# Kernel optimization log

Hardware: AMD Instinct MI355X
Metric: run time of the kernel (lower is better)

The kernel has to match this reference:

```python
import jax, jax.numpy as jnp
import numpy as np

D_MODEL = 1024
NUM_HEADS = 16
D_K = D_MODEL // NUM_HEADS


def setup_inputs() -> dict:
    key = jax.random.key(0)
    ks = jax.random.split(key, 5)
    B, S = 4, 2048
    scale = 1.0 / np.sqrt(D_MODEL)
    return {
        "X": jax.random.normal(ks[0], (B, S, D_MODEL), dtype=jnp.float32),
        "W_q": jax.random.normal(ks[1], (D_MODEL, D_MODEL), dtype=jnp.float32) * scale,
        "W_k": jax.random.normal(ks[2], (D_MODEL, D_MODEL), dtype=jnp.float32) * scale,
        "W_v": jax.random.normal(ks[3], (D_MODEL, D_MODEL), dtype=jnp.float32) * scale,
        "W_h": jax.random.normal(ks[4], (D_MODEL, D_MODEL), dtype=jnp.float32) * scale,
        "b_h": jnp.zeros((D_MODEL,), dtype=jnp.float32),
    }


def reference(X, W_q, W_k, W_v, W_h, b_h):
    # X: [B, S, D] (batch_first=True). Linear weights stored [out, in] as in torch.
    B, S, _ = X.shape

    def split_heads(t):  # [B, S, D] -> [B, H, S, d_k]
        return t.reshape(B, S, NUM_HEADS, D_K).transpose(0, 2, 1, 3)

    Q = split_heads(jnp.einsum('bsd,od->bso', X, W_q))
    K = split_heads(jnp.einsum('bsd,od->bso', X, W_k))
    V = split_heads(jnp.einsum('bsd,od->bso', X, W_v))

    inv_sqrt_dk = jnp.asarray(1.0 / np.sqrt(D_K), dtype=X.dtype)
    scores = jnp.einsum('bhqd,bhkd->bhqk', Q * inv_sqrt_dk, K)  # [B,H,S,S]
    A = jax.nn.softmax(scores, axis=-1)
    H = jnp.einsum('bhqk,bhkd->bhqd', A, V)  # [B,H,S,d_k]
    H_cat = H.transpose(0, 2, 1, 3).reshape(B, S, D_MODEL)
    out = jnp.einsum('bsd,od->bso', H_cat, W_h) + b_h
    return out
```

## Files before the change

kernel.cpp:

```cpp
#include <hip/hip_runtime.h>
#include <hip/hip_bf16.h>


typedef short bf16x8 __attribute__((ext_vector_type(8)));
typedef short bf16x4 __attribute__((ext_vector_type(4)));
typedef float f32x4 __attribute__((ext_vector_type(4)));

#define D_MODEL 1024
#define SEQ     2048
#define BATCH   4
#define NHEAD   16
#define DK      64
#define LOG2E   1.44269504088896340736f
#define QSCALE  (0.125f * LOG2E)

__device__ __forceinline__ bf16x8 load8(const __hip_bfloat16* p) {
    return *reinterpret_cast<const bf16x8*>(p);
}
__device__ __forceinline__ short b16rne(float x) {
    unsigned u = __float_as_uint(x);
    u = (u + 0x7FFFu + ((u >> 16) & 1u)) >> 16;
    return (short)u;
}
__device__ __forceinline__ unsigned cvt_pk_bf16(float lo, float hi) {
    unsigned d;
    asm("v_cvt_pk_bf16_f32 %0, %1, %2" : "=v"(d) : "v"(lo), "v"(hi));
    return d;
}
__device__ __forceinline__ bf16x8 cvt8(const float* p) {
    f32x4 a = *reinterpret_cast<const f32x4*>(p);
    f32x4 b = *reinterpret_cast<const f32x4*>(p + 4);
    union { unsigned u[4]; bf16x8 v; } r;
    r.u[0] = cvt_pk_bf16(a[0], a[1]);
    r.u[1] = cvt_pk_bf16(a[2], a[3]);
    r.u[2] = cvt_pk_bf16(b[0], b[1]);
    r.u[3] = cvt_pk_bf16(b[2], b[3]);
    return r.v;
}
__device__ __forceinline__ void gld_lds16(const __hip_bfloat16* g, __hip_bfloat16* l) {
    __builtin_amdgcn_global_load_lds(
        (const __attribute__((address_space(1))) unsigned int*)g,
        (__attribute__((address_space(3))) unsigned int*)l, 16, 0, 0);
}

#define NX8 1048576
#define NW8 131072
__global__ __launch_bounds__(256) void cvt_all(
    const float* __restrict__ X,  const float* __restrict__ Wq,
    const float* __restrict__ Wk, const float* __restrict__ Wv,
    const float* __restrict__ Wh,
    __hip_bfloat16* __restrict__ Xb, __hip_bfloat16* __restrict__ Wqkv,
    __hip_bfloat16* __restrict__ Whb)
{
    int g = blockIdx.x * 256 + threadIdx.x;
    const float* src;
    __hip_bfloat16* dst;
    if (g < NX8) {
        src = X + (size_t)g * 8;
        dst = Xb + (size_t)g * 8;
    } else {
        int t = g - NX8;
        int r = t >> 17;
        int off = t & (NW8 - 1);
        const float* s0 = (r == 0) ? Wq : (r == 1) ? Wk : (r == 2) ? Wv : Wh;
        src = s0 + (size_t)off * 8;
        dst = ((r < 3) ? (Wqkv + (size_t)r * NW8 * 8) : Whb) + (size_t)off * 8;
    }
    *reinterpret_cast<bf16x8*>(dst) = cvt8(src);
}

__global__ __launch_bounds__(256) void qkv_gemm128(
    const __hip_bfloat16* __restrict__ Xb,
    const __hip_bfloat16* __restrict__ Wqkv,
    __hip_bfloat16* __restrict__ Qo,
    __hip_bfloat16* __restrict__ Ko,
    __hip_bfloat16* __restrict__ Vto)
{
    __shared__ __align__(16) __hip_bfloat16 At[128 * 32];
    __shared__ __align__(16) __hip_bfloat16 Bt[128 * 32];

    const int tid  = threadIdx.x;
    const int wave = tid >> 6, lane = tid & 63;
    const int l15  = lane & 15, quad = lane >> 4;
    const int wm   = wave >> 1, wn = wave & 1;
    const int bm0  = blockIdx.y * 128;
    const int bn0  = blockIdx.x * 128;

    const int srow = wave * 16 + (lane >> 2);
    const int scol = ((lane & 3) ^ ((lane >> 3) & 3)) * 8;
    const __hip_bfloat16* gA = Xb   + (size_t)(bm0 + srow) * 1024 + scol;
    const __hip_bfloat16* gB = Wqkv + (size_t)(bn0 + srow) * 1024 + scol;
    __hip_bfloat16* lA = At + wave * 512;
    __hip_bfloat16* lB = Bt + wave * 512;

    const int rsw = (l15 >> 1) & 3;

    f32x4 acc[4][4];
    #pragma unroll
    for (int i = 0; i < 4; ++i)
        #pragma unroll
        for (int j = 0; j < 4; ++j) acc[i][j] = (f32x4){0.f, 0.f, 0.f, 0.f};

    for (int k0 = 0; k0 < 1024; k0 += 32) {
        gld_lds16(gA + k0,                      lA);
        gld_lds16(gA + (size_t)64 * 1024 + k0,  lA + 2048);
        gld_lds16(gB + k0,                      lB);
        gld_lds16(gB + (size_t)64 * 1024 + k0,  lB + 2048);
        __syncthreads();

        bf16x8 af[4], bfr[4];
        #pragma unroll
        for (int i = 0; i < 4; ++i)
            af[i] = load8(At + (wm * 64 + i * 16 + l15) * 32 + ((quad ^ rsw) * 8));
        #pragma unroll
        for (int j = 0; j < 4; ++j)
            bfr[j] = load8(Bt + (wn * 64 + j * 16 + l15) * 32 + ((quad ^ rsw) * 8));
        #pragma unroll
        for (int i = 0; i < 4; ++i)
            #pragma unroll
            for (int j = 0; j < 4; ++j)
                acc[i][j] = __builtin_amdgcn_mfma_f32_16x16x32_bf16(af[i], bfr[j], acc[i][j], 0, 0, 0);
        __syncthreads();
    }

    const int z = bn0 >> 10;
    #pragma unroll
    for (int j = 0; j < 4; ++j) {
        int n  = bn0 + wn * 64 + j * 16 + l15;
        int nn = n & 1023;
        int h  = nn >> 6, d = nn & 63;
        #pragma unroll
        for (int i = 0; i < 4; ++i) {
            int m0 = bm0 + wm * 64 + i * 16 + quad * 4;
            int b  = m0 >> 11, s0 = m0 & 2047;
            if (z == 2) {
                uint2 pv;
                pv.x = cvt_pk_bf16(acc[i][j][0], acc[i][j][1]);
                pv.y = cvt_pk_bf16(acc[i][j][2], acc[i][j][3]);
                *reinterpret_cast<uint2*>(
                    &Vto[((size_t)((b << 4) + h) * DK + d) * SEQ + s0]) = pv;
            } else {
                #pragma unroll
                for (int r = 0; r < 4; ++r) {
                    float val = acc[i][j][r];
                    short v;
                    if (z == 0) v = b16rne(val * QSCALE); else v = b16rne(val);
                    __hip_bfloat16 bv = *reinterpret_cast<__hip_bfloat16*>(&v);
                    if (z == 0)
                        Qo[((size_t)((b << 4) + h) * SEQ + (s0 + r)) * DK + d] = bv;
                    else
                        Ko[((size_t)((b << 4) + h) * SEQ + (s0 + r)) * DK + d] = bv;
                }
            }
        }
    }
}

__global__ __launch_bounds__(256, 4) void flash_attn(
    const __hip_bfloat16* __restrict__ Q,
    const __hip_bfloat16* __restrict__ K,
    const __hip_bfloat16* __restrict__ Vt,
    __hip_bfloat16* __restrict__ H)
{
    __shared__ __align__(16) __hip_bfloat16 Kt[2][64 * 64];
    __shared__ __align__(16) __hip_bfloat16 Vs[64 * 64];
    __shared__ __align__(16) __hip_bfloat16 Plds[4][2][16][64];

    const int w    = threadIdx.x >> 6;
    const int lane = threadIdx.x & 63;
    const int l15  = lane & 15;
    const int quad = lane >> 4;
    const int x7   = l15 & 7;
    const int bh   = blockIdx.x & 63;
    const int b    = bh >> 4, h = bh & 15;
    const int q0   = (blockIdx.x >> 6) * 128 + w * 32;

    const __hip_bfloat16* Qb = Q  + (size_t)bh * SEQ * DK;
    const __hip_bfloat16* Kb = K  + (size_t)bh * SEQ * DK;
    const __hip_bfloat16* Vb = Vt + (size_t)bh * DK * SEQ;

    const int srsub = lane >> 3;
    const int sseg  = (lane & 7) ^ srsub;
    const int krow0 = w * 16 + srsub;
    const __hip_bfloat16* gK0 = Kb + (size_t)krow0 * DK + sseg * 8;
    const __hip_bfloat16* gK1 = Kb + (size_t)(krow0 + 8) * DK + sseg * 8;
    const __hip_bfloat16* gV0 = Vb + (size_t)krow0 * SEQ + sseg * 8;
    const __hip_bfloat16* gV1 = Vb + (size_t)(krow0 + 8) * SEQ + sseg * 8;
    __hip_bfloat16* lV0 = Vs + (w * 16) * 64;
    __hip_bfloat16* lV1 = Vs + (w * 16 + 8) * 64;

    bf16x8 qf[2][2];
    #pragma unroll
    for (int m = 0; m < 2; ++m)
        #pragma unroll
        for (int dh = 0; dh < 2; ++dh)
            qf[m][dh] = load8(Qb + (size_t)(q0 + m * 16 + l15) * DK + dh * 32 + quad * 8);

    bf16x8 onesf;
    #pragma unroll
    for (int j = 0; j < 8; ++j) onesf[j] = (short)0x3F80;

    f32x4 o[2][4];
    #pragma unroll
    for (int m = 0; m < 2; ++m)
        #pragma unroll
        for (int t = 0; t < 4; ++t) o[m][t] = (f32x4){0.f, 0.f, 0.f, 0.f};
    f32x4 lacc[2] = {{0.f,0.f,0.f,0.f}, {0.f,0.f,0.f,0.f}};

    gld_lds16(gK0, &Kt[0][(w * 16) * 64]);
    gld_lds16(gK1, &Kt[0][(w * 16 + 8) * 64]);
    __syncthreads();

    int cb = 0;
    for (int kv = 0; kv < SEQ; kv += 64) {
        const int nb  = cb ^ 1;
        const int kvn = (kv + 64) & (SEQ - 1);

        gld_lds16(gV0 + kv, lV0);
        gld_lds16(gV1 + kv, lV1);
        gld_lds16(gK0 + (size_t)kvn * DK, &Kt[nb][(w * 16) * 64]);
        gld_lds16(gK1 + (size_t)kvn * DK, &Kt[nb][(w * 16 + 8) * 64]);

        f32x4 s[2][4];
        __builtin_amdgcn_s_setprio(1);
        #pragma unroll
        for (int kvh = 0; kvh < 4; ++kvh) {
            bf16x8 kf0 = load8(&Kt[cb][(kvh * 16 + l15) * 64 + ((0 + quad) ^ x7) * 8]);
            bf16x8 kf1 = load8(&Kt[cb][(kvh * 16 + l15) * 64 + ((4 + quad) ^ x7) * 8]);
            #pragma unroll
            for (int m = 0; m < 2; ++m) {
                f32x4 c = {0.f, 0.f, 0.f, 0.f};
                c = __builtin_amdgcn_mfma_f32_16x16x32_bf16(kf0, qf[m][0], c, 0, 0, 0);
                c = __builtin_amdgcn_mfma_f32_16x16x32_bf16(kf1, qf[m][1], c, 0, 0, 0);
                s[m][kvh] = c;
            }
        }
        __builtin_amdgcn_s_setprio(0);

        bf16x8 pf[2][2];
        {
            uint2 pr[2][4];
            #pragma unroll
            for (int m = 0; m < 2; ++m)
                #pragma unroll
                for (int kvh = 0; kvh < 4; ++kvh) {
                    float e0 = __builtin_amdgcn_exp2f(s[m][kvh][0]);
                    float e1 = __builtin_amdgcn_exp2f(s[m][kvh][1]);
                    float e2 = __builtin_amdgcn_exp2f(s[m][kvh][2]);
                    float e3 = __builtin_amdgcn_exp2f(s[m][kvh][3]);
                    pr[m][kvh].x = cvt_pk_bf16(e0, e1);
                    pr[m][kvh].y = cvt_pk_bf16(e2, e3);
                }
            #pragma unroll
            for (int m = 0; m < 2; ++m)
                #pragma unroll
                for (int kvh = 0; kvh < 4; ++kvh)
                    *reinterpret_cast<uint2*>(
                        &Plds[w][m][l15][(kvh * 16 + quad * 4) ^ (x7 << 3)]) = pr[m][kvh];
            asm volatile("s_waitcnt lgkmcnt(0)" ::: "memory");
            #pragma unroll
            for (int m = 0; m < 2; ++m) {
                pf[m][0] = load8(&Plds[w][m][l15][(quad * 8) ^ (x7 << 3)]);
                pf[m][1] = load8(&Plds[w][m][l15][(32 + quad * 8) ^ (x7 << 3)]);
            }
            #pragma unroll
            for (int m = 0; m < 2; ++m) {
                lacc[m] = __builtin_amdgcn_mfma_f32_16x16x32_bf16(pf[m][0], onesf, lacc[m], 0, 0, 0);
                lacc[m] = __builtin_amdgcn_mfma_f32_16x16x32_bf16(pf[m][1], onesf, lacc[m], 0, 0, 0);
            }
        }

        asm volatile("s_waitcnt vmcnt(2)" ::: "memory");
        __builtin_amdgcn_s_barrier();
        asm volatile("" ::: "memory");

        __builtin_amdgcn_s_setprio(1);
        #pragma unroll
        for (int t = 0; t < 4; ++t) {
            bf16x8 vf0 = load8(&Vs[(t * 16 + l15) * 64 + ((0 + quad) ^ x7) * 8]);
            bf16x8 vf1 = load8(&Vs[(t * 16 + l15) * 64 + ((4 + quad) ^ x7) * 8]);
            #pragma unroll
            for (int m = 0; m < 2; ++m) {
                o[m][t] = __builtin_amdgcn_mfma_f32_16x16x32_bf16(pf[m][0], vf0, o[m][t], 0, 0, 0);
                o[m][t] = __builtin_amdgcn_mfma_f32_16x16x32_bf16(pf[m][1], vf1, o[m][t], 0, 0, 0);
            }
        }
        __builtin_amdgcn_s_setprio(0);

        __syncthreads();
        cb = nb;
    }

    #pragma unroll
    for (int m = 0; m < 2; ++m) {
        float inv_l[4];
        #pragma unroll
        for (int r = 0; r < 4; ++r) inv_l[r] = 1.0f / lacc[m][r];
        #pragma unroll
        for (int t = 0; t < 4; ++t) {
            int d = h * 64 + t * 16 + l15;
            #pragma unroll
            for (int r = 0; r < 4; ++r) {
                int sidx = q0 + m * 16 + quad * 4 + r;
                short hv = b16rne(o[m][t][r] * inv_l[r]);
                H[((size_t)b * SEQ + sidx) * D_MODEL + d] =
                    *reinterpret_cast<__hip_bfloat16*>(&hv);
            }
        }
    }
}

__global__ __launch_bounds__(256) void out_gemm128(
    const __hip_bfloat16* __restrict__ Hc,
    const __hip_bfloat16* __restrict__ Whb,
    const float* __restrict__ bias,
    float* __restrict__ out)
{
    __shared__ __align__(16) __hip_bfloat16 At[128 * 32];
    __shared__ __align__(16) __hip_bfloat16 Bt[128 * 32];

    const int tid  = threadIdx.x;
    const int wave = tid >> 6, lane = tid & 63;
    const int l15  = lane & 15, quad = lane >> 4;
    const int wm   = wave >> 1, wn = wave & 1;
    const int bm0  = blockIdx.y * 128;
    const int bn0  = blockIdx.x * 128;

    const int srow = wave * 16 + (lane >> 2);
    const int scol = ((lane & 3) ^ ((lane >> 3) & 3)) * 8;
    const __hip_bfloat16* gA = Hc  + (size_t)(bm0 + srow) * 1024 + scol;
    const __hip_bfloat16* gB = Whb + (size_t)(bn0 + srow) * 1024 + scol;
    __hip_bfloat16* lA = At + wave * 512;
    __hip_bfloat16* lB = Bt + wave * 512;

    const int rsw = (l15 >> 1) & 3;

    f32x4 acc[4][4];
    #pragma unroll
    for (int i = 0; i < 4; ++i)
        #pragma unroll
        for (int j = 0; j < 4; ++j) acc[i][j] = (f32x4){0.f, 0.f, 0.f, 0.f};

    for (int k0 = 0; k0 < 1024; k0 += 32) {
        gld_lds16(gA + k0,                      lA);
        gld_lds16(gA + (size_t)64 * 1024 + k0,  lA + 2048);
        gld_lds16(gB + k0,                      lB);
        gld_lds16(gB + (size_t)64 * 1024 + k0,  lB + 2048);
        __syncthreads();

        bf16x8 af[4], bfr[4];
        #pragma unroll
        for (int i = 0; i < 4; ++i)
            af[i] = load8(At + (wm * 64 + i * 16 + l15) * 32 + ((quad ^ rsw) * 8));
        #pragma unroll
        for (int j = 0; j < 4; ++j)
            bfr[j] = load8(Bt + (wn * 64 + j * 16 + l15) * 32 + ((quad ^ rsw) * 8));
        #pragma unroll
        for (int i = 0; i < 4; ++i)
            #pragma unroll
            for (int j = 0; j < 4; ++j)
                acc[i][j] = __builtin_amdgcn_mfma_f32_16x16x32_bf16(af[i], bfr[j], acc[i][j], 0, 0, 0);
        __syncthreads();
    }

    #pragma unroll
    for (int j = 0; j < 4; ++j) {
        int n = bn0 + wn * 64 + j * 16 + l15;
        float bv = bias[n];
        #pragma unroll
        for (int i = 0; i < 4; ++i) {
            #pragma unroll
            for (int r = 0; r < 4; ++r) {
                int m = bm0 + wm * 64 + i * 16 + quad * 4 + r;
                out[(size_t)m * D_MODEL + n] = acc[i][j][r] + bv;
            }
        }
    }
}

extern "C" void kernel_launch(void* const* d_in, const int* in_sizes, int n_in,
                              void* d_out, int out_size, void* d_ws, size_t ws_size,
                              hipStream_t stream) {
    const float* X  = (const float*)d_in[0];
    const float* Wq = (const float*)d_in[1];
    const float* Wk = (const float*)d_in[2];
    const float* Wv = (const float*)d_in[3];
    const float* Wh = (const float*)d_in[4];
    const float* bh = (const float*)d_in[5];
    float* out = (float*)d_out;

    const size_t NX = (size_t)BATCH * SEQ * D_MODEL;
    const size_t NW = (size_t)D_MODEL * D_MODEL;

    __hip_bfloat16* Xb   = (__hip_bfloat16*)d_ws;
    __hip_bfloat16* Hw   = Xb;
    __hip_bfloat16* Wqkv = Xb + NX;
    __hip_bfloat16* Whb  = Wqkv + 3 * NW;
    __hip_bfloat16* Qw   = Whb + NW;
    __hip_bfloat16* Kw   = Qw + NX;
    __hip_bfloat16* Vtw  = Kw + NX;

    cvt_all<<<(NX8 + 4 * NW8) / 256, 256, 0, stream>>>(
        X, Wq, Wk, Wv, Wh, Xb, Wqkv, Whb);

    qkv_gemm128<<<dim3(3 * D_MODEL / 128, (BATCH * SEQ) / 128), 256, 0, stream>>>(
        Xb, Wqkv, Qw, Kw, Vtw);
    flash_attn<<<(SEQ / 128) * BATCH * NHEAD, 256, 0, stream>>>(Qw, Kw, Vtw, Hw);
    out_gemm128<<<dim3(D_MODEL / 128, (BATCH * SEQ) / 128), 256, 0, stream>>>(
        Hw, Whb, bh, out);
}
```

Baseline: 278.2 us.

## Double-buffer LDS tiles in QKV and output projection GEMMs

Both projection GEMMs now keep two LDS buffers for the A and B tiles. Each iteration issues the global-to-LDS loads for the next K slice, then waits with vmcnt only for the current slice before the barrier. This is meant to overlap global memory latency with MFMA work, where before every step stalled on its own loads. It doubles the LDS footprint per block, which can lower occupancy, and relies on hand-placed waitcnt counts being correct.

```diff
diff --git a/kernel.cpp b/kernel.cpp
--- a/kernel.cpp
+++ b/kernel.cpp
@@ -76,8 +76,8 @@
     __hip_bfloat16* __restrict__ Ko,
     __hip_bfloat16* __restrict__ Vto)
 {
-    __shared__ __align__(16) __hip_bfloat16 At[128 * 32];
-    __shared__ __align__(16) __hip_bfloat16 Bt[128 * 32];
+    __shared__ __align__(16) __hip_bfloat16 At[2][128 * 32];
+    __shared__ __align__(16) __hip_bfloat16 Bt[2][128 * 32];
 
     const int tid  = threadIdx.x;
     const int wave = tid >> 6, lane = tid & 63;
@@ -90,8 +90,7 @@
     const int scol = ((lane & 3) ^ ((lane >> 3) & 3)) * 8;
     const __hip_bfloat16* gA = Xb   + (size_t)(bm0 + srow) * 1024 + scol;
     const __hip_bfloat16* gB = Wqkv + (size_t)(bn0 + srow) * 1024 + scol;
-    __hip_bfloat16* lA = At + wave * 512;
-    __hip_bfloat16* lB = Bt + wave * 512;
+    const int lofs = wave * 512;
 
     const int rsw = (l15 >> 1) & 3;
 
@@ -101,26 +100,41 @@
         #pragma unroll
         for (int j = 0; j < 4; ++j) acc[i][j] = (f32x4){0.f, 0.f, 0.f, 0.f};
 
+    gld_lds16(gA,                      At[0] + lofs);
+    gld_lds16(gA + (size_t)64 * 1024,  At[0] + lofs + 2048);
+    gld_lds16(gB,                      Bt[0] + lofs);
+    gld_lds16(gB + (size_t)64 * 1024,  Bt[0] + lofs + 2048);
+
+    int cb = 0;
     for (int k0 = 0; k0 < 1024; k0 += 32) {
-        gld_lds16(gA + k0,                      lA);
-        gld_lds16(gA + (size_t)64 * 1024 + k0,  lA + 2048);
-        gld_lds16(gB + k0,                      lB);
-        gld_lds16(gB + (size_t)64 * 1024 + k0,  lB + 2048);
-        __syncthreads();
+        const int nb = cb ^ 1;
+        if (k0 < 1024 - 32) {
+            const int k1 = k0 + 32;
+            gld_lds16(gA + k1,                      At[nb] + lofs);
+            gld_lds16(gA + (size_t)64 * 1024 + k1,  At[nb] + lofs + 2048);
+            gld_lds16(gB + k1,                      Bt[nb] + lofs);
+            gld_lds16(gB + (size_t)64 * 1024 + k1,  Bt[nb] + lofs + 2048);
+            asm volatile("s_waitcnt vmcnt(4)" ::: "memory");
+        } else {
+            asm volatile("s_waitcnt vmcnt(0)" ::: "memory");
+        }
+        __builtin_amdgcn_s_barrier();
+        asm volatile("" ::: "memory");
 
         bf16x8 af[4], bfr[4];
         #pragma unroll
         for (int i = 0; i < 4; ++i)
-            af[i] = load8(At + (wm * 64 + i * 16 + l15) * 32 + ((quad ^ rsw) * 8));
+            af[i] = load8(At[cb] + (wm * 64 + i * 16 + l15) * 32 + ((quad ^ rsw) * 8));
         #pragma unroll
         for (int j = 0; j < 4; ++j)
-            bfr[j] = load8(Bt + (wn * 64 + j * 16 + l15) * 32 + ((quad ^ rsw) * 8));
+            bfr[j] = load8(Bt[cb] + (wn * 64 + j * 16 + l15) * 32 + ((quad ^ rsw) * 8));
         #pragma unroll
         for (int i = 0; i < 4; ++i)
             #pragma unroll
             for (int j = 0; j < 4; ++j)
                 acc[i][j] = __builtin_amdgcn_mfma_f32_16x16x32_bf16(af[i], bfr[j], acc[i][j], 0, 0, 0);
         __syncthreads();
+        cb = nb;
     }
 
     const int z = bn0 >> 10;
@@ -316,8 +330,8 @@
     const float* __restrict__ bias,
     float* __restrict__ out)
 {
-    __shared__ __align__(16) __hip_bfloat16 At[128 * 32];
-    __shared__ __align__(16) __hip_bfloat16 Bt[128 * 32];
+    __shared__ __align__(16) __hip_bfloat16 At[2][128 * 32];
+    __shared__ __align__(16) __hip_bfloat16 Bt[2][128 * 32];
 
     const int tid  = threadIdx.x;
     const int wave = tid >> 6, lane = tid & 63;
@@ -330,8 +344,7 @@
     const int scol = ((lane & 3) ^ ((lane >> 3) & 3)) * 8;
     const __hip_bfloat16* gA = Hc  + (size_t)(bm0 + srow) * 1024 + scol;
     const __hip_bfloat16* gB = Whb + (size_t)(bn0 + srow) * 1024 + scol;
-    __hip_bfloat16* lA = At + wave * 512;
-    __hip_bfloat16* lB = Bt + wave * 512;
+    const int lofs = wave * 512;
 
     const int rsw = (l15 >> 1) & 3;
 
@@ -341,26 +354,41 @@
         #pragma unroll
         for (int j = 0; j < 4; ++j) acc[i][j] = (f32x4){0.f, 0.f, 0.f, 0.f};
 
+    gld_lds16(gA,                      At[0] + lofs);
+    gld_lds16(gA + (size_t)64 * 1024,  At[0] + lofs + 2048);
+    gld_lds16(gB,                      Bt[0] + lofs);
+    gld_lds16(gB + (size_t)64 * 1024,  Bt[0] + lofs + 2048);
+
+    int cb = 0;
     for (int k0 = 0; k0 < 1024; k0 += 32) {
-        gld_lds16(gA + k0,                      lA);
-        gld_lds16(gA + (size_t)64 * 1024 + k0,  lA + 2048);
-        gld_lds16(gB + k0,                      lB);
-        gld_lds16(gB + (size_t)64 * 1024 + k0,  lB + 2048);
-        __syncthreads();
+        const int nb = cb ^ 1;
+        if (k0 < 1024 - 32) {
+            const int k1 = k0 + 32;
+            gld_lds16(gA + k1,                      At[nb] + lofs);
+            gld_lds16(gA + (size_t)64 * 1024 + k1,  At[nb] + lofs + 2048);
+            gld_lds16(gB + k1,                      Bt[nb] + lofs);
+            gld_lds16(gB + (size_t)64 * 1024 + k1,  Bt[nb] + lofs + 2048);
+            asm volatile("s_waitcnt vmcnt(4)" ::: "memory");
+        } else {
+            asm volatile("s_waitcnt vmcnt(0)" ::: "memory");
+        }
+        __builtin_amdgcn_s_barrier();
+        asm volatile("" ::: "memory");
 
         bf16x8 af[4], bfr[4];
         #pragma unroll
         for (int i = 0; i < 4; ++i)
-            af[i] = load8(At + (wm * 64 + i * 16 + l15) * 32 + ((quad ^ rsw) * 8));
+            af[i] = load8(At[cb] + (wm * 64 + i * 16 + l15) * 32 + ((quad ^ rsw) * 8));
         #pragma unroll
         for (int j = 0; j < 4; ++j)
-            bfr[j] = load8(Bt + (wn * 64 + j * 16 + l15) * 32 + ((quad ^ rsw) * 8));
+            bfr[j] = load8(Bt[cb] + (wn * 64 + j * 16 + l15) * 32 + ((quad ^ rsw) * 8));
         #pragma unroll
         for (int i = 0; i < 4; ++i)
             #pragma unroll
             for (int j = 0; j < 4; ++j)
                 acc[i][j] = __builtin_amdgcn_mfma_f32_16x16x32_bf16(af[i], bfr[j], acc[i][j], 0, 0, 0);
         __syncthreads();
+        cb = nb;
     }
 
     #pragma unroll
```

New measurement: 267.1 us. 4.0% less time.
